# Kernel tuning notes

Measured on AMD Instinct MI355X. Metric: run time of the kernel, lower is better.

The kernel has to match this reference:

```python
import jax, jax.numpy as jnp
import numpy as np

NUM_HEADS = 16
ROPE_BASE = 10000.0


def _rope_cos_sin(seq_len, head_dim, dtype):
    # freqs for the half-dim; original caches cat(freqs, freqs) and then applies
    # the rotation per-half, which is equivalent to using the half-size tables.
    inv_freq = 1.0 / (ROPE_BASE ** (jnp.arange(0, head_dim, 2, dtype=jnp.float32) / head_dim))
    t = jnp.arange(seq_len, dtype=jnp.float32)
    freqs = jnp.einsum('i,j->ij', t, inv_freq)  # [S, hd/2]
    return jnp.cos(freqs).astype(dtype), jnp.sin(freqs).astype(dtype)


def _apply_rotary(x, cos, sin):
    # x: [B, H, S, hd]; cos/sin: [S, hd/2] broadcast over B, H
    half = x.shape[-1] // 2
    x1, x2 = x[..., :half], x[..., half:]
    return jnp.concatenate([x1 * cos - x2 * sin, x2 * cos + x1 * sin], axis=-1)


def setup_inputs() -> dict:
    key = jax.random.key(0)
    ks = jax.random.split(key, 5)
    D = 2048
    B, S = 2, 2048
    std = 1.0 / np.sqrt(D)
    return {
        'x': jax.random.normal(ks[0], (B, S, D), dtype=jnp.float32),
        'Wq': jax.random.normal(ks[1], (D, D), dtype=jnp.float32) * std,
        'Wk': jax.random.normal(ks[2], (D, D), dtype=jnp.float32) * std,
        'Wv': jax.random.normal(ks[3], (D, D), dtype=jnp.float32) * std,
        'Wo': jax.random.normal(ks[4], (D, D), dtype=jnp.float32) * std,
    }


def reference(x, Wq, Wk, Wv, Wo):
    B, S, D = x.shape
    H = NUM_HEADS
    hd = D // H
    scale = hd ** -0.5

    def proj(W):  # torch Linear: y = x @ W.T -> [B, H, S, hd]
        return (x @ W.T).reshape(B, S, H, hd).transpose(0, 2, 1, 3)

    q, k, v = proj(Wq), proj(Wk), proj(Wv)

    cos, sin = _rope_cos_sin(S, hd, x.dtype)
    q = _apply_rotary(q, cos, sin)
    k = _apply_rotary(k, cos, sin)

    scores = jnp.einsum('bhqd,bhkd->bhqk', q, k) * scale  # full O(S^2) scores
    attn = jax.nn.softmax(scores, axis=-1)
    out = jnp.einsum('bhqk,bhkd->bhqd', attn, v)
    out = out.transpose(0, 2, 1, 3).reshape(B, S, D)
    return out @ Wo.T
```

## Files before the change

kernel.cpp:

```cpp
#include <hip/hip_runtime.h>
#include <cstdint>

typedef __attribute__((ext_vector_type(8))) short bf16x8;
typedef __attribute__((ext_vector_type(4))) float f32x4;
typedef __attribute__((ext_vector_type(16))) float f32x16;

__device__ inline unsigned short f2bf(float f) {
  uint32_t u = __float_as_uint(f);
  uint32_t lsb = (u >> 16) & 1u;
  u += 0x7fffu + lsb;
  return (unsigned short)(u >> 16);
}
__device__ inline float bf2f(unsigned short b) {
  return __uint_as_float(((uint32_t)b) << 16);
}
__device__ inline uint32_t cvt_pk_bf16(float lo, float hi) {
  uint32_t r;
  asm volatile("v_cvt_pk_bf16_f32 %0, %1, %2" : "=v"(r) : "v"(lo), "v"(hi));
  return r;
}

#define GLOAD16(gp, lp)                                                        \
  __builtin_amdgcn_global_load_lds(                                            \
      (const __attribute__((address_space(1))) void*)(gp),                     \
      (__attribute__((address_space(3))) void*)(lp), 16, 0, 0)

__global__ void cvt_all(const float* __restrict__ x, const float* __restrict__ wq,
                        const float* __restrict__ wk, const float* __restrict__ wv,
                        const float* __restrict__ wos, unsigned short* __restrict__ xb,
                        unsigned short* __restrict__ wqkv,
                        unsigned short* __restrict__ wo) {
  size_t e = ((size_t)blockIdx.x * 256 + threadIdx.x) * 4;
  const float* src;
  unsigned short* dst;
  if (e < 8388608) {
    src = x + e;
    dst = xb + e;
  } else {
    size_t r = e - 8388608;
    int k = (int)(r >> 22);
    size_t off = r & 4194303;
    if (k == 0) { src = wq + off; dst = wqkv + r; }
    else if (k == 1) { src = wk + off; dst = wqkv + r; }
    else if (k == 2) { src = wv + off; dst = wqkv + r; }
    else { src = wos + off; dst = wo + off; }
  }
  float4 v = *(const float4*)src;
  unsigned short o[4] = {f2bf(v.x), f2bf(v.y), f2bf(v.z), f2bf(v.w)};
  *(uint64_t*)dst = *(const uint64_t*)o;
}

__global__ void rope_table_k(float* __restrict__ ctab, float* __restrict__ stab) {
  int i = blockIdx.x * 256 + threadIdx.x;
  int s = i >> 6, j = i & 63;
  float invf = expf(-(float)j * (9.210340371976184f / 64.0f));
  float ang = (float)s * invf;
  ctab[i] = cosf(ang);
  stab[i] = sinf(ang);
}

__global__ void rope_apply_k(unsigned short* __restrict__ qb,
                             unsigned short* __restrict__ kb,
                             const float* __restrict__ ctab,
                             const float* __restrict__ stab) {
  int row = blockIdx.x * 16 + (threadIdx.x >> 4);
  int c = (threadIdx.x & 15) * 4;
  int s = row & 2047;
  int bh = (row >> 11) & 31;
  int isK = row >> 16;
  unsigned short* base = isK ? kb : qb;
  float qs = isK ? 1.0f : (0.08838834764831845f * 1.4426950408889634f);
  unsigned short* p = base + ((size_t)bh * 2048 + s) * 128;
  float4 cv = *(const float4*)(ctab + s * 64 + c);
  float4 sv = *(const float4*)(stab + s * 64 + c);
  union { unsigned short u[4]; uint64_t q; } a, b2, oa, ob;
  a.q = *(const uint64_t*)(p + c);
  b2.q = *(const uint64_t*)(p + 64 + c);
  float cc[4] = {cv.x, cv.y, cv.z, cv.w};
  float ss[4] = {sv.x, sv.y, sv.z, sv.w};
#pragma unroll
  for (int i = 0; i < 4; i++) {
    float x1 = bf2f(a.u[i]), x2 = bf2f(b2.u[i]);
    oa.u[i] = f2bf((x1 * cc[i] - x2 * ss[i]) * qs);
    ob.u[i] = f2bf((x2 * cc[i] + x1 * ss[i]) * qs);
  }
  *(uint64_t*)(p + c) = oa.q;
  *(uint64_t*)(p + 64 + c) = ob.q;
}

__global__ void transpose_v_k(const unsigned short* __restrict__ v,
                              unsigned short* __restrict__ vt) {
  __shared__ unsigned short tile[64][72];
  int bh = blockIdx.x, st = blockIdx.y, dt = blockIdx.z;
  const unsigned short* src = v + ((size_t)bh * 2048 + st * 64) * 128 + dt * 64;
  unsigned short* dst = vt + ((size_t)bh * 128 + dt * 64) * 2048 + st * 64;
  int t = threadIdx.x;
  int r = t >> 2, c0 = (t & 3) * 16;
  *(bf16x8*)&tile[r][c0] = *(const bf16x8*)(src + (size_t)r * 128 + c0);
  *(bf16x8*)&tile[r][c0 + 8] = *(const bf16x8*)(src + (size_t)r * 128 + c0 + 8);
  __syncthreads();
  unsigned short o[16];
#pragma unroll
  for (int i = 0; i < 16; i++) o[i] = tile[c0 + i][r];
  *(bf16x8*)(dst + (size_t)r * 2048 + c0) = *(const bf16x8*)&o[0];
  *(bf16x8*)(dst + (size_t)r * 2048 + c0 + 8) = *(const bf16x8*)&o[8];
}

template <int EPI>
__global__ __launch_bounds__(256, 2) void gemm_bt(
    const unsigned short* __restrict__ A, const unsigned short* __restrict__ Bm,
    float* __restrict__ Cf, int M, int N, int K) {
  __shared__ unsigned short sA[128 * 32];
  __shared__ unsigned short sB[128 * 32];
  const int t = threadIdx.x;
  const int w = t >> 6, l = t & 63;
  const int wr = w >> 1, wc = w & 1;
  const int bm = blockIdx.x * 128, bn = blockIdx.y * 128;
  const int lr = l & 15, lg = l >> 4;
  f32x4 acc[4][4] = {};

  const int srow = w * 16 + (l >> 2);
  const int sseg = (l & 3) * 8;
  const unsigned short* ga = A + (size_t)(bm + srow) * K + sseg;
  const unsigned short* gb = Bm + (size_t)(bn + srow) * K + sseg;
  unsigned short* lA = sA + w * 512 + l * 8;
  unsigned short* lB = sB + w * 512 + l * 8;

  for (int kt = 0; kt < K; kt += 32) {
    __syncthreads();
    GLOAD16(ga + kt, lA);
    GLOAD16(ga + kt + (size_t)64 * K, lA + 2048);
    GLOAD16(gb + kt, lB);
    GLOAD16(gb + kt + (size_t)64 * K, lB + 2048);
    __syncthreads();
    bf16x8 af[4], bfv[4];
#pragma unroll
    for (int m = 0; m < 4; m++)
      af[m] = *(const bf16x8*)(sA + (wr * 64 + m * 16 + lr) * 32 + lg * 8);
#pragma unroll
    for (int n = 0; n < 4; n++)
      bfv[n] = *(const bf16x8*)(sB + (wc * 64 + n * 16 + lr) * 32 + lg * 8);
#pragma unroll
    for (int m = 0; m < 4; m++)
#pragma unroll
      for (int n = 0; n < 4; n++)
        acc[m][n] = __builtin_amdgcn_mfma_f32_16x16x32_bf16(af[m], bfv[n],
                                                            acc[m][n], 0, 0, 0);
  }

#pragma unroll
  for (int m = 0; m < 4; m++) {
#pragma unroll
    for (int n = 0; n < 4; n++) {
      int gm0 = bm + wr * 64 + m * 16 + lg * 4;
      int gn = bn + wc * 64 + n * 16 + lr;
#pragma unroll
      for (int j = 0; j < 4; j++) {
        Cf[(size_t)(gm0 + j) * N + gn] = acc[m][n][j];
      }
    }
  }
}

template <int EPI>
__global__ __launch_bounds__(512, 1) void gemm256(
    const unsigned short* __restrict__ A, const unsigned short* __restrict__ Bm,
    float* __restrict__ Cf, unsigned short* __restrict__ q_out,
    unsigned short* __restrict__ k_out, unsigned short* __restrict__ v_out,
    int M, int N, int K, int nbm) {
  __shared__ unsigned short sA[2][2][256 * 32];
  __shared__ unsigned short sB[2][2][192 * 32];

  const int t = threadIdx.x;
  const int w = t >> 6, l = t & 63;
  const int wr = w >> 2, wc = w & 3;
  const int lr = l & 15, lg = l >> 4;
  const int gsw = (lg ^ ((lr >> 1) & 3)) * 8;

  const int cpx = gridDim.x >> 3;
  const int bid = blockIdx.x;
  const int swz = (bid & 7) * cpx + (bid >> 3);
  const int bm = (swz % nbm) * 256, bn = (swz / nbm) * 192;

  f32x4 acc[8][3] = {};

  const unsigned short* Ab = A + (size_t)bm * K;
  const unsigned short* Bb = Bm + (size_t)bn * K;

#define STAGE_A(plane, koff)                                                   \
  do {                                                                         \
    _Pragma("unroll") for (int i = 0; i < 2; i++) {                            \
      int g = i * 512 + t;                                                     \
      int row = g >> 2, c = g & 3;                                             \
      GLOAD16(Ab + (size_t)row * K + (koff) + ((c ^ ((row >> 1) & 3)) * 8),    \
              (plane) + g * 8);                                                \
    }                                                                          \
  } while (0)

#define STAGE_B(plane, koff)                                                   \
  do {                                                                         \
    _Pragma("unroll") for (int i = 0; i < 3; i++) {                            \
      int g = i * 512 + t;                                                     \
      int kh = (g >= 768) ? 1 : 0;                                             \
      int gr = g - kh * 768;                                                   \
      int row = gr >> 2, c = gr & 3;                                           \
      GLOAD16(Bb + (size_t)row * K + (koff) + kh * 32 +                        \
                  ((c ^ ((row >> 1) & 3)) * 8),                                \
              (plane) + g * 8);                                                \
    }                                                                          \
  } while (0)

  STAGE_B(&sB[0][0][0], 0);
  STAGE_A(&sA[0][0][0], 0);
  STAGE_A(&sA[0][1][0], 32);
  asm volatile("s_waitcnt vmcnt(2)" ::: "memory");
  __builtin_amdgcn_s_barrier();

  const int NT = K >> 6;
  for (int t2 = 0; t2 < NT; ++t2) {
    const int db = t2 & 1, dn = db ^ 1;
    const int kt = (t2 + 1 < NT ? t2 + 1 : t2) * 64;
    bf16x8 a[4], a2[4], b[3];

#pragma unroll
    for (int mf = 0; mf < 4; mf++)
      a[mf] = *(const bf16x8*)&sA[db][0][(wr * 128 + mf * 16 + lr) * 32 + gsw];
#pragma unroll
    for (int nf = 0; nf < 3; nf++)
      b[nf] = *(const bf16x8*)&sB[db][0][(wc * 48 + nf * 16 + lr) * 32 + gsw];
    STAGE_B(&sB[dn][0][0], kt);
    __builtin_amdgcn_s_barrier();
    asm volatile("s_waitcnt lgkmcnt(0)" ::: "memory");
    __builtin_amdgcn_sched_barrier(0);
    __builtin_amdgcn_s_setprio(1);
#pragma unroll
    for (int mf = 0; mf < 4; mf++)
#pragma unroll
      for (int nf = 0; nf < 3; nf++)
        acc[mf][nf] = __builtin_amdgcn_mfma_f32_16x16x32_bf16(a[mf], b[nf],
                                                              acc[mf][nf], 0, 0, 0);
    __builtin_amdgcn_s_setprio(0);
    __builtin_amdgcn_s_barrier();

#pragma unroll
    for (int mf = 0; mf < 4; mf++)
      a2[mf] = *(const bf16x8*)&sA[db][0][(wr * 128 + (mf + 4) * 16 + lr) * 32 + gsw];
    STAGE_A(&sA[dn][0][0], kt);
    __builtin_amdgcn_s_barrier();
    asm volatile("s_waitcnt lgkmcnt(0)" ::: "memory");
    __builtin_amdgcn_sched_barrier(0);
    __builtin_amdgcn_s_setprio(1);
#pragma unroll
    for (int mf = 0; mf < 4; mf++)
#pragma unroll
      for (int nf = 0; nf < 3; nf++)
        acc[mf + 4][nf] = __builtin_amdgcn_mfma_f32_16x16x32_bf16(
            a2[mf], b[nf], acc[mf + 4][nf], 0, 0, 0);
    __builtin_amdgcn_s_setprio(0);
    asm volatile("s_waitcnt vmcnt(5)" ::: "memory");
    __builtin_amdgcn_s_barrier();

#pragma unroll
    for (int mf = 0; mf < 4; mf++)
      a[mf] = *(const bf16x8*)&sA[db][1][(wr * 128 + mf * 16 + lr) * 32 + gsw];
#pragma unroll
    for (int nf = 0; nf < 3; nf++)
      b[nf] = *(const bf16x8*)&sB[db][1][(wc * 48 + nf * 16 + lr) * 32 + gsw];
    STAGE_A(&sA[dn][1][0], kt + 32);
    __builtin_amdgcn_s_barrier();
    asm volatile("s_waitcnt lgkmcnt(0)" ::: "memory");
    __builtin_amdgcn_sched_barrier(0);
    __builtin_amdgcn_s_setprio(1);
#pragma unroll
    for (int mf = 0; mf < 4; mf++)
#pragma unroll
      for (int nf = 0; nf < 3; nf++)
        acc[mf][nf] = __builtin_amdgcn_mfma_f32_16x16x32_bf16(a[mf], b[nf],
                                                              acc[mf][nf], 0, 0, 0);
    __builtin_amdgcn_s_setprio(0);
    __builtin_amdgcn_s_barrier();

#pragma unroll
    for (int mf = 0; mf < 4; mf++)
      a2[mf] = *(const bf16x8*)&sA[db][1][(wr * 128 + (mf + 4) * 16 + lr) * 32 + gsw];
    __builtin_amdgcn_s_barrier();
    asm volatile("s_waitcnt lgkmcnt(0)" ::: "memory");
    __builtin_amdgcn_sched_barrier(0);
    __builtin_amdgcn_s_setprio(1);
#pragma unroll
    for (int mf = 0; mf < 4; mf++)
#pragma unroll
      for (int nf = 0; nf < 3; nf++)
        acc[mf + 4][nf] = __builtin_amdgcn_mfma_f32_16x16x32_bf16(
            a2[mf], b[nf], acc[mf + 4][nf], 0, 0, 0);
    __builtin_amdgcn_s_setprio(0);
    asm volatile("s_waitcnt vmcnt(2)" ::: "memory");
    __builtin_amdgcn_s_barrier();
  }

#pragma unroll
  for (int mf = 0; mf < 8; mf++) {
#pragma unroll
    for (int nf = 0; nf < 3; nf++) {
      int gm0 = bm + wr * 128 + mf * 16 + lg * 4;
      int gn = bn + wc * 48 + nf * 16 + lr;
#pragma unroll
      for (int j = 0; j < 4; j++) {
        float v = acc[mf][nf][j];
        int gm = gm0 + j;
        if (EPI == 0) {
          Cf[(size_t)gm * N + gn] = v;
        } else {
          int which = gn >> 11, rem = gn & 2047;
          int h = rem >> 7, d = rem & 127;
          int b = gm >> 11, s = gm & 2047;
          unsigned short* dst = which == 0 ? q_out : (which == 1 ? k_out : v_out);
          dst[(((size_t)(b * 16 + h)) * 2048 + s) * 128 + d] = f2bf(v);
        }
      }
    }
  }
}

__global__ __launch_bounds__(256, 2) void attn_k(
    const unsigned short* __restrict__ Q, const unsigned short* __restrict__ K,
    const unsigned short* __restrict__ Vt, unsigned short* __restrict__ ctx) {
  __shared__ unsigned short sK[2][64 * 128];
  __shared__ unsigned short sV[2][128 * 64];

  const int qt = blockIdx.x, bh = blockIdx.y;
  const int t = threadIdx.x;
  const int w = t >> 6, l = t & 63;
  const int lq = l & 31;
  const int h5 = l >> 5;
  const int b = bh >> 4, hh = bh & 15;
  const int q0 = qt * 128 + w * 32;
  const unsigned short* Qp = Q + ((size_t)bh * 2048 + q0) * 128;
  const unsigned short* Kbh = K + (size_t)bh * 2048 * 128;
  const unsigned short* Vbh = Vt + (size_t)bh * 128 * 2048;

  int gko[4], gvo[4];
#pragma unroll
  for (int i = 0; i < 4; i++) {
    int p = i * 256 + t;
    int rK = p >> 4, cK = p & 15;
    gko[i] = rK * 128 + ((cK ^ (rK & 7)) * 8);
    int rV = p >> 3, cV = p & 7;
    gvo[i] = rV * 2048 + ((cV ^ (rV & 7)) * 8);
  }

  bf16x8 qf[8];
#pragma unroll
  for (int st = 0; st < 8; st++)
    qf[st] = *(const bf16x8*)(Qp + lq * 128 + st * 16 + h5 * 8);

  f32x16 o[4];
#pragma unroll
  for (int db = 0; db < 4; db++) o[db] = (f32x16)0.0f;
  float m_r = -1e30f, l_r = 0.0f;

#define STAGE_KV(buf, kv)                                                      \
  do {                                                                         \
    _Pragma("unroll") for (int i = 0; i < 4; i++)                              \
        GLOAD16(Kbh + (size_t)(kv)*128 + gko[i],                               \
                sK[buf] + (i * 256 + t) * 8);                                  \
    _Pragma("unroll") for (int i = 0; i < 4; i++)                              \
        GLOAD16(Vbh + (size_t)(kv) + gvo[i], sV[buf] + (i * 256 + t) * 8);     \
  } while (0)

  STAGE_KV(0, 0);
  __syncthreads();

  for (int it = 0; it < 32; ++it) {
    const int cur = it & 1;
    if (it < 31) STAGE_KV(cur ^ 1, (it + 1) * 64);

    const char* kbuf = (const char*)sK[cur];
    const char* vbuf = (const char*)sV[cur];

    f32x16 s2[2];
#pragma unroll
    for (int kb2 = 0; kb2 < 2; kb2++) {
      s2[kb2] = (f32x16)0.0f;
      const int rr = kb2 * 32 + lq;
      const int swzz = (rr & 7) << 4;
#pragma unroll
      for (int st = 0; st < 8; st++) {
        bf16x8 kf = *(const bf16x8*)(kbuf + rr * 256 + ((st * 32 + h5 * 16) ^ swzz));
        s2[kb2] = __builtin_amdgcn_mfma_f32_32x32x16_bf16(kf, qf[st], s2[kb2], 0, 0, 0);
      }
    }

    float sm[32];
#pragma unroll
    for (int kb2 = 0; kb2 < 2; kb2++)
#pragma unroll
      for (int r = 0; r < 16; r++) sm[kb2 * 16 + r] = s2[kb2][r];

    float tmax = sm[0];
#pragma unroll
    for (int i = 1; i < 32; i++) tmax = fmaxf(tmax, sm[i]);
    tmax = fmaxf(tmax, __shfl_xor(tmax, 32));

    if (!__all(tmax <= m_r + 8.0f)) {
      float m_new = fmaxf(m_r, tmax);
      float fac = exp2f(m_r - m_new);
      l_r *= fac;
      float fo[16];
#pragma unroll
      for (int r = 0; r < 16; r++)
        fo[r] = __shfl(fac, (r & 3) + 8 * (r >> 2) + 4 * h5);
#pragma unroll
      for (int db = 0; db < 4; db++)
#pragma unroll
        for (int r = 0; r < 16; r++) o[db][r] *= fo[r];
      m_r = m_new;
    }

    float psum = 0.0f;
#pragma unroll
    for (int i = 0; i < 32; i++) {
      sm[i] = exp2f(sm[i] - m_r);
      psum += sm[i];
    }
    psum += __shfl_xor(psum, 32);
    l_r += psum;

    uint32_t wAp[2][4], wBp[2][4];
#pragma unroll
    for (int kb2 = 0; kb2 < 2; kb2++)
#pragma unroll
      for (int rq = 0; rq < 4; rq++) {
        wAp[kb2][rq] = cvt_pk_bf16(sm[kb2 * 16 + rq * 4 + 0], sm[kb2 * 16 + rq * 4 + 1]);
        wBp[kb2][rq] = cvt_pk_bf16(sm[kb2 * 16 + rq * 4 + 2], sm[kb2 * 16 + rq * 4 + 3]);
      }

#pragma unroll
    for (int st = 0; st < 4; st++) {
      const int kb2 = st >> 1, p2 = (st & 1) * 2;
      uint32_t keepA = h5 ? wAp[kb2][p2 + 1] : wAp[kb2][p2];
      uint32_t keepB = h5 ? wBp[kb2][p2 + 1] : wBp[kb2][p2];
      uint32_t sendA = h5 ? wAp[kb2][p2] : wAp[kb2][p2 + 1];
      uint32_t sendB = h5 ? wBp[kb2][p2] : wBp[kb2][p2 + 1];
      uint32_t partA = __shfl_xor(sendA, 32);
      uint32_t partB = __shfl_xor(sendB, 32);
      union {
        uint32_t u[4];
        bf16x8 v;
      } pu;
      pu.u[0] = h5 ? partA : keepA;
      pu.u[1] = h5 ? partB : keepB;
      pu.u[2] = h5 ? keepA : partA;
      pu.u[3] = h5 ? keepB : partB;
#pragma unroll
      for (int db = 0; db < 4; db++) {
        const int rv = db * 32 + lq;
        const int swzz = (rv & 7) << 4;
        bf16x8 vb = *(const bf16x8*)(vbuf + rv * 128 + ((st * 32 + h5 * 16) ^ swzz));
        o[db] = __builtin_amdgcn_mfma_f32_32x32x16_bf16(pu.v, vb, o[db], 0, 0, 0);
      }
    }
    __syncthreads();
  }

  float inv = 1.0f / l_r;
  float io[16];
#pragma unroll
  for (int r = 0; r < 16; r++)
    io[r] = __shfl(inv, (r & 3) + 8 * (r >> 2) + 4 * h5);
#pragma unroll
  for (int db = 0; db < 4; db++) {
#pragma unroll
    for (int r = 0; r < 16; r++) {
      int s = q0 + (r & 3) + 8 * (r >> 2) + 4 * h5;
      ctx[((size_t)(b * 2048 + s)) * 2048 + hh * 128 + db * 32 + lq] =
          f2bf(o[db][r] * io[r]);
    }
  }
}

extern "C" void kernel_launch(void* const* d_in, const int* in_sizes, int n_in,
                              void* d_out, int out_size, void* d_ws,
                              size_t ws_size, hipStream_t stream) {
  const float* x = (const float*)d_in[0];
  const float* Wq = (const float*)d_in[1];
  const float* Wk = (const float*)d_in[2];
  const float* Wv = (const float*)d_in[3];
  const float* Wo = (const float*)d_in[4];
  float* out = (float*)d_out;

  const size_t BS = 4096;
  const size_t D = 2048;

  char* p = (char*)d_ws;
  unsigned short* xb = (unsigned short*)p;   p += BS * D * 2;
  unsigned short* wqkv = (unsigned short*)p; p += 3 * D * D * 2;
  unsigned short* wo = (unsigned short*)p;   p += D * D * 2;
  unsigned short* qb = (unsigned short*)p;   p += BS * D * 2;
  unsigned short* kb = (unsigned short*)p;   p += BS * D * 2;
  unsigned short* vb = (unsigned short*)p;   p += BS * D * 2;
  float* ctab = (float*)p;                   p += 2048 * 64 * 4;
  float* stab = (float*)p;                   p += 2048 * 64 * 4;
  unsigned short* vt = wqkv;
  unsigned short* ctx = xb;

  cvt_all<<<24576, 256, 0, stream>>>(x, Wq, Wk, Wv, Wo, xb, wqkv, wo);
  rope_table_k<<<512, 256, 0, stream>>>(ctab, stab);

  gemm256<1><<<512, 512, 0, stream>>>(xb, wqkv, nullptr, qb, kb, vb, 4096, 6144,
                                      2048, 16);
  rope_apply_k<<<8192, 256, 0, stream>>>(qb, kb, ctab, stab);
  transpose_v_k<<<dim3(32, 32, 2), 256, 0, stream>>>(vb, vt);
  attn_k<<<dim3(16, 32), 256, 0, stream>>>(qb, kb, vt, ctx);
  gemm_bt<0><<<dim3(32, 16), 256, 0, stream>>>(ctx, wo, out, 4096, 2048, 2048);
}
```

Before: 293.1 us.

## Double per-wave query rows in attention and swizzle LDS in output GEMM

The attention kernel now has each wave handle 64 query rows as two 32-row sub-tiles that share every K and V fragment read from LDS. This halves the grid and the total K/V traffic per query. Launch bounds drop to one block per SIMD set to make room for the extra registers. Separately, the output-projection GEMM XOR-swizzles its LDS layout to reduce bank conflicts on fragment reads. The risks are lower occupancy (256 blocks on 256 CUs) and register pressure from the doubled accumulators and softmax state.

```diff
diff --git a/kernel.cpp b/kernel.cpp
--- a/kernel.cpp
+++ b/kernel.cpp
@@ -117,10 +117,11 @@
   const int wr = w >> 1, wc = w & 1;
   const int bm = blockIdx.x * 128, bn = blockIdx.y * 128;
   const int lr = l & 15, lg = l >> 4;
+  const int gsw = (lg ^ ((lr >> 1) & 3)) * 8;
   f32x4 acc[4][4] = {};
 
   const int srow = w * 16 + (l >> 2);
-  const int sseg = (l & 3) * 8;
+  const int sseg = ((l & 3) ^ ((l >> 3) & 3)) * 8;
   const unsigned short* ga = A + (size_t)(bm + srow) * K + sseg;
   const unsigned short* gb = Bm + (size_t)(bn + srow) * K + sseg;
   unsigned short* lA = sA + w * 512 + l * 8;
@@ -136,10 +137,10 @@
     bf16x8 af[4], bfv[4];
 #pragma unroll
     for (int m = 0; m < 4; m++)
-      af[m] = *(const bf16x8*)(sA + (wr * 64 + m * 16 + lr) * 32 + lg * 8);
+      af[m] = *(const bf16x8*)(sA + (wr * 64 + m * 16 + lr) * 32 + gsw);
 #pragma unroll
     for (int n = 0; n < 4; n++)
-      bfv[n] = *(const bf16x8*)(sB + (wc * 64 + n * 16 + lr) * 32 + lg * 8);
+      bfv[n] = *(const bf16x8*)(sB + (wc * 64 + n * 16 + lr) * 32 + gsw);
 #pragma unroll
     for (int m = 0; m < 4; m++)
 #pragma unroll
@@ -322,7 +323,7 @@
   }
 }
 
-__global__ __launch_bounds__(256, 2) void attn_k(
+__global__ __launch_bounds__(256, 1) void attn_k(
     const unsigned short* __restrict__ Q, const unsigned short* __restrict__ K,
     const unsigned short* __restrict__ Vt, unsigned short* __restrict__ ctx) {
   __shared__ unsigned short sK[2][64 * 128];
@@ -334,7 +335,7 @@
   const int lq = l & 31;
   const int h5 = l >> 5;
   const int b = bh >> 4, hh = bh & 15;
-  const int q0 = qt * 128 + w * 32;
+  const int q0 = qt * 256 + w * 64;
   const unsigned short* Qp = Q + ((size_t)bh * 2048 + q0) * 128;
   const unsigned short* Kbh = K + (size_t)bh * 2048 * 128;
   const unsigned short* Vbh = Vt + (size_t)bh * 128 * 2048;
@@ -349,15 +350,20 @@
     gvo[i] = rV * 2048 + ((cV ^ (rV & 7)) * 8);
   }
 
-  bf16x8 qf[8];
-#pragma unroll
-  for (int st = 0; st < 8; st++)
-    qf[st] = *(const bf16x8*)(Qp + lq * 128 + st * 16 + h5 * 8);
-
-  f32x16 o[4];
-#pragma unroll
-  for (int db = 0; db < 4; db++) o[db] = (f32x16)0.0f;
-  float m_r = -1e30f, l_r = 0.0f;
+  bf16x8 qfA[8], qfB[8];
+#pragma unroll
+  for (int st = 0; st < 8; st++) {
+    qfA[st] = *(const bf16x8*)(Qp + lq * 128 + st * 16 + h5 * 8);
+    qfB[st] = *(const bf16x8*)(Qp + (lq + 32) * 128 + st * 16 + h5 * 8);
+  }
+
+  f32x16 oA[4], oB[4];
+#pragma unroll
+  for (int db = 0; db < 4; db++) {
+    oA[db] = (f32x16)0.0f;
+    oB[db] = (f32x16)0.0f;
+  }
+  float mA = -1e30f, lA_ = 0.0f, mB = -1e30f, lB_ = 0.0f;
 
 #define STAGE_KV(buf, kv)                                                      \
   do {                                                                         \
@@ -378,103 +384,173 @@
     const char* kbuf = (const char*)sK[cur];
     const char* vbuf = (const char*)sV[cur];
 
-    f32x16 s2[2];
+    f32x16 sA2[2], sB2[2];
 #pragma unroll
     for (int kb2 = 0; kb2 < 2; kb2++) {
-      s2[kb2] = (f32x16)0.0f;
+      sA2[kb2] = (f32x16)0.0f;
+      sB2[kb2] = (f32x16)0.0f;
       const int rr = kb2 * 32 + lq;
       const int swzz = (rr & 7) << 4;
 #pragma unroll
       for (int st = 0; st < 8; st++) {
         bf16x8 kf = *(const bf16x8*)(kbuf + rr * 256 + ((st * 32 + h5 * 16) ^ swzz));
-        s2[kb2] = __builtin_amdgcn_mfma_f32_32x32x16_bf16(kf, qf[st], s2[kb2], 0, 0, 0);
-      }
-    }
-
-    float sm[32];
-#pragma unroll
-    for (int kb2 = 0; kb2 < 2; kb2++)
-#pragma unroll
-      for (int r = 0; r < 16; r++) sm[kb2 * 16 + r] = s2[kb2][r];
-
-    float tmax = sm[0];
-#pragma unroll
-    for (int i = 1; i < 32; i++) tmax = fmaxf(tmax, sm[i]);
-    tmax = fmaxf(tmax, __shfl_xor(tmax, 32));
-
-    if (!__all(tmax <= m_r + 8.0f)) {
-      float m_new = fmaxf(m_r, tmax);
-      float fac = exp2f(m_r - m_new);
-      l_r *= fac;
-      float fo[16];
-#pragma unroll
-      for (int r = 0; r < 16; r++)
-        fo[r] = __shfl(fac, (r & 3) + 8 * (r >> 2) + 4 * h5);
-#pragma unroll
-      for (int db = 0; db < 4; db++)
-#pragma unroll
-        for (int r = 0; r < 16; r++) o[db][r] *= fo[r];
-      m_r = m_new;
-    }
-
-    float psum = 0.0f;
-#pragma unroll
-    for (int i = 0; i < 32; i++) {
-      sm[i] = exp2f(sm[i] - m_r);
-      psum += sm[i];
-    }
-    psum += __shfl_xor(psum, 32);
-    l_r += psum;
-
-    uint32_t wAp[2][4], wBp[2][4];
-#pragma unroll
-    for (int kb2 = 0; kb2 < 2; kb2++)
-#pragma unroll
-      for (int rq = 0; rq < 4; rq++) {
-        wAp[kb2][rq] = cvt_pk_bf16(sm[kb2 * 16 + rq * 4 + 0], sm[kb2 * 16 + rq * 4 + 1]);
-        wBp[kb2][rq] = cvt_pk_bf16(sm[kb2 * 16 + rq * 4 + 2], sm[kb2 * 16 + rq * 4 + 3]);
-      }
+        sA2[kb2] = __builtin_amdgcn_mfma_f32_32x32x16_bf16(kf, qfA[st], sA2[kb2], 0, 0, 0);
+        sB2[kb2] = __builtin_amdgcn_mfma_f32_32x32x16_bf16(kf, qfB[st], sB2[kb2], 0, 0, 0);
+      }
+    }
+
+    uint32_t wApA[2][4], wBpA[2][4], wApB[2][4], wBpB[2][4];
+    {
+      float sm[32];
+#pragma unroll
+      for (int kb2 = 0; kb2 < 2; kb2++)
+#pragma unroll
+        for (int r = 0; r < 16; r++) sm[kb2 * 16 + r] = sA2[kb2][r];
+      float tmax = sm[0];
+#pragma unroll
+      for (int i = 1; i < 32; i++) tmax = fmaxf(tmax, sm[i]);
+      tmax = fmaxf(tmax, __shfl_xor(tmax, 32));
+      if (!__all(tmax <= mA + 8.0f)) {
+        float m_new = fmaxf(mA, tmax);
+        float fac = exp2f(mA - m_new);
+        lA_ *= fac;
+        float fo[16];
+#pragma unroll
+        for (int r = 0; r < 16; r++)
+          fo[r] = __shfl(fac, (r & 3) + 8 * (r >> 2) + 4 * h5);
+#pragma unroll
+        for (int db = 0; db < 4; db++)
+#pragma unroll
+          for (int r = 0; r < 16; r++) oA[db][r] *= fo[r];
+        mA = m_new;
+      }
+      float psum = 0.0f;
+#pragma unroll
+      for (int i = 0; i < 32; i++) {
+        sm[i] = exp2f(sm[i] - mA);
+        psum += sm[i];
+      }
+      psum += __shfl_xor(psum, 32);
+      lA_ += psum;
+#pragma unroll
+      for (int kb2 = 0; kb2 < 2; kb2++)
+#pragma unroll
+        for (int rq = 0; rq < 4; rq++) {
+          wApA[kb2][rq] = cvt_pk_bf16(sm[kb2 * 16 + rq * 4 + 0], sm[kb2 * 16 + rq * 4 + 1]);
+          wBpA[kb2][rq] = cvt_pk_bf16(sm[kb2 * 16 + rq * 4 + 2], sm[kb2 * 16 + rq * 4 + 3]);
+        }
+    }
+    {
+      float sm[32];
+#pragma unroll
+      for (int kb2 = 0; kb2 < 2; kb2++)
+#pragma unroll
+        for (int r = 0; r < 16; r++) sm[kb2 * 16 + r] = sB2[kb2][r];
+      float tmax = sm[0];
+#pragma unroll
+      for (int i = 1; i < 32; i++) tmax = fmaxf(tmax, sm[i]);
+      tmax = fmaxf(tmax, __shfl_xor(tmax, 32));
+      if (!__all(tmax <= mB + 8.0f)) {
+        float m_new = fmaxf(mB, tmax);
+        float fac = exp2f(mB - m_new);
+        lB_ *= fac;
+        float fo[16];
+#pragma unroll
+        for (int r = 0; r < 16; r++)
+          fo[r] = __shfl(fac, (r & 3) + 8 * (r >> 2) + 4 * h5);
+#pragma unroll
+        for (int db = 0; db < 4; db++)
+#pragma unroll
+          for (int r = 0; r < 16; r++) oB[db][r] *= fo[r];
+        mB = m_new;
+      }
+      float psum = 0.0f;
+#pragma unroll
+      for (int i = 0; i < 32; i++) {
+        sm[i] = exp2f(sm[i] - mB);
+        psum += sm[i];
+      }
+      psum += __shfl_xor(psum, 32);
+      lB_ += psum;
+#pragma unroll
+      for (int kb2 = 0; kb2 < 2; kb2++)
+#pragma unroll
+        for (int rq = 0; rq < 4; rq++) {
+          wApB[kb2][rq] = cvt_pk_bf16(sm[kb2 * 16 + rq * 4 + 0], sm[kb2 * 16 + rq * 4 + 1]);
+          wBpB[kb2][rq] = cvt_pk_bf16(sm[kb2 * 16 + rq * 4 + 2], sm[kb2 * 16 + rq * 4 + 3]);
+        }
+    }
 
 #pragma unroll
     for (int st = 0; st < 4; st++) {
       const int kb2 = st >> 1, p2 = (st & 1) * 2;
-      uint32_t keepA = h5 ? wAp[kb2][p2 + 1] : wAp[kb2][p2];
-      uint32_t keepB = h5 ? wBp[kb2][p2 + 1] : wBp[kb2][p2];
-      uint32_t sendA = h5 ? wAp[kb2][p2] : wAp[kb2][p2 + 1];
-      uint32_t sendB = h5 ? wBp[kb2][p2] : wBp[kb2][p2 + 1];
-      uint32_t partA = __shfl_xor(sendA, 32);
-      uint32_t partB = __shfl_xor(sendB, 32);
-      union {
-        uint32_t u[4];
-        bf16x8 v;
-      } pu;
-      pu.u[0] = h5 ? partA : keepA;
-      pu.u[1] = h5 ? partB : keepB;
-      pu.u[2] = h5 ? keepA : partA;
-      pu.u[3] = h5 ? keepB : partB;
+      union { uint32_t u[4]; bf16x8 v; } puA, puB;
+      {
+        uint32_t keepA = h5 ? wApA[kb2][p2 + 1] : wApA[kb2][p2];
+        uint32_t keepB = h5 ? wBpA[kb2][p2 + 1] : wBpA[kb2][p2];
+        uint32_t sendA = h5 ? wApA[kb2][p2] : wApA[kb2][p2 + 1];
+        uint32_t sendB = h5 ? wBpA[kb2][p2] : wBpA[kb2][p2 + 1];
+        uint32_t partA = __shfl_xor(sendA, 32);
+        uint32_t partB = __shfl_xor(sendB, 32);
+        puA.u[0] = h5 ? partA : keepA;
+        puA.u[1] = h5 ? partB : keepB;
+        puA.u[2] = h5 ? keepA : partA;
+        puA.u[3] = h5 ? keepB : partB;
+      }
+      {
+        uint32_t keepA = h5 ? wApB[kb2][p2 + 1] : wApB[kb2][p2];
+        uint32_t keepB = h5 ? wBpB[kb2][p2 + 1] : wBpB[kb2][p2];
+        uint32_t sendA = h5 ? wApB[kb2][p2] : wApB[kb2][p2 + 1];
+        uint32_t sendB = h5 ? wBpB[kb2][p2] : wBpB[kb2][p2 + 1];
+        uint32_t partA = __shfl_xor(sendA, 32);
+        uint32_t partB = __shfl_xor(sendB, 32);
+        puB.u[0] = h5 ? partA : keepA;
+        puB.u[1] = h5 ? partB : keepB;
+        puB.u[2] = h5 ? keepA : partA;
+        puB.u[3] = h5 ? keepB : partB;
+      }
 #pragma unroll
       for (int db = 0; db < 4; db++) {
         const int rv = db * 32 + lq;
         const int swzz = (rv & 7) << 4;
         bf16x8 vb = *(const bf16x8*)(vbuf + rv * 128 + ((st * 32 + h5 * 16) ^ swzz));
-        o[db] = __builtin_amdgcn_mfma_f32_32x32x16_bf16(pu.v, vb, o[db], 0, 0, 0);
+        oA[db] = __builtin_amdgcn_mfma_f32_32x32x16_bf16(puA.v, vb, oA[db], 0, 0, 0);
+        oB[db] = __builtin_amdgcn_mfma_f32_32x32x16_bf16(puB.v, vb, oB[db], 0, 0, 0);
       }
     }
     __syncthreads();
   }
 
-  float inv = 1.0f / l_r;
-  float io[16];
-#pragma unroll
-  for (int r = 0; r < 16; r++)
-    io[r] = __shfl(inv, (r & 3) + 8 * (r >> 2) + 4 * h5);
-#pragma unroll
-  for (int db = 0; db < 4; db++) {
-#pragma unroll
-    for (int r = 0; r < 16; r++) {
-      int s = q0 + (r & 3) + 8 * (r >> 2) + 4 * h5;
-      ctx[((size_t)(b * 2048 + s)) * 2048 + hh * 128 + db * 32 + lq] =
-          f2bf(o[db][r] * io[r]);
+  {
+    float inv = 1.0f / lA_;
+    float io[16];
+#pragma unroll
+    for (int r = 0; r < 16; r++)
+      io[r] = __shfl(inv, (r & 3) + 8 * (r >> 2) + 4 * h5);
+#pragma unroll
+    for (int db = 0; db < 4; db++) {
+#pragma unroll
+      for (int r = 0; r < 16; r++) {
+        int s = q0 + (r & 3) + 8 * (r >> 2) + 4 * h5;
+        ctx[((size_t)(b * 2048 + s)) * 2048 + hh * 128 + db * 32 + lq] =
+            f2bf(oA[db][r] * io[r]);
+      }
+    }
+  }
+  {
+    float inv = 1.0f / lB_;
+    float io[16];
+#pragma unroll
+    for (int r = 0; r < 16; r++)
+      io[r] = __shfl(inv, (r & 3) + 8 * (r >> 2) + 4 * h5);
+#pragma unroll
+    for (int db = 0; db < 4; db++) {
+#pragma unroll
+      for (int r = 0; r < 16; r++) {
+        int s = q0 + 32 + (r & 3) + 8 * (r >> 2) + 4 * h5;
+        ctx[((size_t)(b * 2048 + s)) * 2048 + hh * 128 + db * 32 + lq] =
+            f2bf(oB[db][r] * io[r]);
+      }
     }
   }
 }
@@ -511,6 +587,6 @@
                                       2048, 16);
   rope_apply_k<<<8192, 256, 0, stream>>>(qb, kb, ctab, stab);
   transpose_v_k<<<dim3(32, 32, 2), 256, 0, stream>>>(vb, vt);
-  attn_k<<<dim3(16, 32), 256, 0, stream>>>(qb, kb, vt, ctx);
+  attn_k<<<dim3(8, 32), 256, 0, stream>>>(qb, kb, vt, ctx);
   gemm_bt<0><<<dim3(32, 16), 256, 0, stream>>>(ctx, wo, out, 4096, 2048, 2048);
 }
```

New measurement: 324.7 us. 1.11x slower.
